# Optimization experiments

Hardware: AMD Instinct MI355X
Metric: run time of the kernel (lower is better)

## Reference

```python
import jax, jax.numpy as jnp
import numpy as np

B, N_HEADS, F_TOK = 8, 12, 768
GRID_H, GRID_W = 32, 32
N_TOK = 1 + GRID_H * GRID_W  # 1025 (readout token + patches)
F_HEAD = F_TOK // N_HEADS    # 64
NUM_DIST = (2 * GRID_H - 1) * (2 * GRID_W - 1) + 3  # 3972


def _build_relpos_index(gh, gw):
    # BEiT-style relative position index with 3 extra slots for the readout token
    coords = np.stack(np.meshgrid(np.arange(gh), np.arange(gw), indexing='ij'))  # (2, gh, gw)
    flat = coords.reshape(2, -1)                                                 # (2, gh*gw)
    rel = flat[:, :, None] - flat[:, None, :]                                    # (2, P, P)
    rel = rel.transpose(1, 2, 0).astype(np.int64)                                # (P, P, 2)
    rel[:, :, 0] += gh - 1
    rel[:, :, 1] += gw - 1
    rel[:, :, 0] *= 2 * gw - 1
    rpi = rel.sum(-1)                                                            # (P, P)
    n = 1 + gh * gw
    nd = (2 * gh - 1) * (2 * gw - 1) + 3
    idx = np.zeros((n, n), dtype=np.int32)
    idx[1:, 1:] = rpi
    idx[0, :] = nd - 3  # readout -> all
    idx[:, 0] = nd - 2  # all -> readout
    idx[0, 0] = nd - 1  # readout -> readout
    return idx


def setup_inputs() -> dict:
    key = jax.random.key(0)
    ks = jax.random.split(key, 7)
    tokens = jax.random.normal(ks[0], (B, N_TOK, F_TOK), dtype=jnp.float32)
    qkv_w = jax.random.normal(ks[1], (3 * F_TOK, F_TOK), dtype=jnp.float32) * 0.02
    q_bias = jax.random.normal(ks[2], (1, N_HEADS, 1, F_HEAD), dtype=jnp.float32) * 0.02
    v_bias = jax.random.normal(ks[3], (1, N_HEADS, 1, F_HEAD), dtype=jnp.float32) * 0.02
    relpos_table = jax.random.normal(ks[4], (NUM_DIST, N_HEADS), dtype=jnp.float32) * 0.02
    proj_w = jax.random.normal(ks[5], (F_TOK, F_TOK), dtype=jnp.float32) * 0.02
    proj_b = jax.random.normal(ks[6], (F_TOK,), dtype=jnp.float32) * 0.02
    relpos_index = jnp.asarray(_build_relpos_index(GRID_H, GRID_W))  # (N, N) int32
    return {
        'tokens': tokens, 'qkv_w': qkv_w, 'q_bias': q_bias, 'v_bias': v_bias,
        'relpos_table': relpos_table, 'proj_w': proj_w, 'proj_b': proj_b,
        'relpos_index': relpos_index, 'patch_h': GRID_H, 'patch_w': GRID_W,
    }


def reference(tokens, qkv_w, q_bias, v_bias, relpos_table, proj_w, proj_b,
              relpos_index, patch_h, patch_w):
    b, n, f_tok = tokens.shape
    # qkv projection (no bias): (B, N, 3F) -> (3, B, H, N, f)
    qkv = tokens @ qkv_w.T
    qkv = qkv.reshape(b, n, 3, N_HEADS, F_HEAD).transpose(2, 0, 3, 1, 4)
    q, k, v = qkv[0], qkv[1], qkv[2]
    q = (q + q_bias) * (F_HEAD ** -0.5)
    v = v + v_bias
    # attention scores: (B, H, N, N)
    attn = jnp.einsum('bhnf,bhmf->bhnm', q, k)
    # relative position bias gather: (N, N, H) -> (H, N, N)
    bias = relpos_table[relpos_index].transpose(2, 0, 1)
    attn = attn + bias[None]
    w = jax.nn.softmax(attn, axis=-1)
    out = jnp.einsum('bhnm,bhmf->bhnf', w, v)
    out = out.transpose(0, 2, 1, 3).reshape(b, n, N_HEADS * F_HEAD)
    return out @ proj_w.T + proj_b
```

## Files before the change

kernel.cpp:

```cpp
#include <hip/hip_runtime.h>

#define B_ 8
#define NH 12
#define NTOK 1025
#define FT 768
#define MROWS (B_*NTOK)
#define NPAD2 1088
#define CH2 34
#define NQT 36
#define NTT 34
#define NRT18 18
#define LOG2E 1.44269504089f

typedef __bf16 bf16x8 __attribute__((ext_vector_type(8)));
typedef __bf16 bf16x2 __attribute__((ext_vector_type(2)));
typedef float floatx4 __attribute__((ext_vector_type(4)));
typedef float floatx16 __attribute__((ext_vector_type(16)));
typedef int intx4 __attribute__((ext_vector_type(4)));

__device__ __forceinline__ void async_ld16(const void* gp, void* lp) {
  __builtin_amdgcn_global_load_lds(
      (const __attribute__((address_space(1))) void*)gp,
      (__attribute__((address_space(3))) void*)lp, 16, 0, 0);
}

__global__ __launch_bounds__(256) void cvt_bf16(const float* __restrict__ src,
                                                __bf16* __restrict__ dst, int n4) {
  int i = blockIdx.x * 256 + threadIdx.x;
  if (i >= n4) return;
  float4 v = ((const float4*)src)[i];
  __bf16 o[4] = {(__bf16)v.x, (__bf16)v.y, (__bf16)v.z, (__bf16)v.w};
  *(uint2*)(dst + 4 * (size_t)i) = *(uint2*)o;
}

__global__ __launch_bounds__(256) void bias_gather_t(
    const int* __restrict__ idx, const float* __restrict__ table,
    __bf16* __restrict__ Bb) {
  const int qt = blockIdx.x, tt = blockIdx.y;
  const int t = threadIdx.x;
  const int lane = t & 63, w = t >> 6;
  const int l31 = lane & 31, hb = lane >> 5;
  int qrow = qt * 32 + l31; if (qrow > NTOK - 1) qrow = NTOK - 1;
  int ids[16]; bool ok[16];
#pragma unroll
  for (int j = 0; j < 16; ++j) {
    const int token = tt * 32 + (j & 3) + 8 * (j >> 2) + 4 * hb;
    ok[j] = token < NTOK;
    ids[j] = ok[j] ? idx[qrow * NTOK + token] : 0;
  }
#pragma unroll
  for (int g = 0; g < 3; ++g) {
    const int h = w + g * 4;
    __bf16 v[16];
#pragma unroll
    for (int j = 0; j < 16; ++j)
      v[j] = ok[j] ? (__bf16)(table[ids[j] * NH + h] * LOG2E) : (__bf16)(-1e30f);
    uint4* dst = (uint4*)(Bb + (((size_t)h * NQT + qt) * NTT + tt) * 1024 + lane * 16);
    dst[0] = ((uint4*)v)[0];
    dst[1] = ((uint4*)v)[1];
  }
}

__device__ __forceinline__ void gemm128_pipe(
    const __bf16* __restrict__ A, const __bf16* __restrict__ W,
    int m0, int n0, int M, __bf16* At, __bf16* Bt, floatx4 acc[4][4]) {
  const int tid = threadIdx.x, wave = tid >> 6, lane = tid & 63;
  const int l = lane & 15, qd = lane >> 4;
  const int wr = wave >> 1, wc = wave & 1;
  const int srow = lane >> 2, sg = lane & 3;
  const int r0 = wave * 32 + srow, r1 = r0 + 16;
  int gm0 = m0 + r0; if (gm0 >= M) gm0 = M - 1;
  int gm1 = m0 + r1; if (gm1 >= M) gm1 = M - 1;
  const int sw0 = (sg ^ (r0 & 3)) * 8;
  const __bf16* gA0 = A + (size_t)gm0 * FT + sw0;
  const __bf16* gA1 = A + (size_t)gm1 * FT + sw0;
  const __bf16* gB0 = W + (size_t)(n0 + r0) * FT + sw0;
  const __bf16* gB1 = W + (size_t)(n0 + r1) * FT + sw0;
  const int woff = wave * 32 * 32;
  const int fsw = (qd ^ (l & 3)) * 8;

  auto issue = [&](int k, int buf) {
    __bf16* a = At + buf * 4096 + woff;
    __bf16* b = Bt + buf * 4096 + woff;
    async_ld16(gA0 + k * 32, a);
    async_ld16(gA1 + k * 32, a + 512);
    async_ld16(gB0 + k * 32, b);
    async_ld16(gB1 + k * 32, b + 512);
  };
  auto step = [&](int buf) {
    __builtin_amdgcn_s_barrier();
    const __bf16* ab = At + buf * 4096;
    const __bf16* bb = Bt + buf * 4096;
    bf16x8 aF[4], bF[4];
#pragma unroll
    for (int t = 0; t < 4; ++t)
      aF[t] = *(const bf16x8*)(ab + (wr * 64 + t * 16 + l) * 32 + fsw);
#pragma unroll
    for (int u = 0; u < 4; ++u)
      bF[u] = *(const bf16x8*)(bb + (wc * 64 + u * 16 + l) * 32 + fsw);
#pragma unroll
    for (int t = 0; t < 4; ++t)
#pragma unroll
      for (int u = 0; u < 4; ++u)
        acc[t][u] = __builtin_amdgcn_mfma_f32_16x16x32_bf16(aF[t], bF[u], acc[t][u], 0, 0, 0);
  };

  issue(0, 0);
  int bk = 0;
  for (int k = 0; k < 23; ++k) {
    int bn = bk + 1; if (bn == 3) bn = 0;
    issue(k + 1, bn);
    __builtin_amdgcn_s_waitcnt(0x0F74);
    step(bk);
    bk = bn;
  }
  __builtin_amdgcn_s_waitcnt(0x0F70);
  step(bk);
}

__global__ __launch_bounds__(256) void qkv_gemm128(
    const __bf16* __restrict__ tokens, const __bf16* __restrict__ qkvw,
    const float* __restrict__ qbias, const float* __restrict__ vbias,
    __bf16* __restrict__ Qb, __bf16* __restrict__ Kc, __bf16* __restrict__ Vc) {
  __shared__ __bf16 At[3 * 4096], Bt[3 * 4096];
  const int u0 = blockIdx.x;
  const int c = u0 & 7, q0 = u0 >> 3;
  const int mi = (q0 / 18) * 8 + c, ni = q0 % 18;
  if (mi >= 65) return;
  const int m0 = mi * 128, n0 = ni * 128;
  const int tid = threadIdx.x, wave = tid >> 6, lane = tid & 63;
  const int l = lane & 15, qd = lane >> 4;
  const int wr = wave >> 1, wc = wave & 1;
  floatx4 acc[4][4];
#pragma unroll
  for (int t = 0; t < 4; ++t)
#pragma unroll
    for (int u = 0; u < 4; ++u) acc[t][u] = (floatx4){0.f, 0.f, 0.f, 0.f};
  gemm128_pipe(tokens, qkvw, m0, n0, MROWS, At, Bt, acc);

  const int which = (n0 / FT);
  const int nrem0 = n0 - which * FT;
#pragma unroll
  for (int u = 0; u < 4; ++u) {
    const int rem = nrem0 + wc * 64 + u * 16 + l;
    const int h = rem >> 6, f = rem & 63;
    const float qb = (which == 0) ? qbias[h * 64 + f] : 0.f;
    const float vb = (which == 2) ? vbias[h * 64 + f] : 0.f;
#pragma unroll
    for (int t = 0; t < 4; ++t) {
#pragma unroll
      for (int r = 0; r < 4; ++r) {
        const int gm = m0 + wr * 64 + t * 16 + qd * 4 + r;
        if (gm >= MROWS) continue;
        const int b = gm / NTOK;
        const int tok = gm - b * NTOK;
        const size_t bh = (size_t)(b * NH + h);
        float v = acc[t][u][r];
        if (which == 0) {
          Qb[(bh * NPAD2 + tok) * 64 + f] = (__bf16)((v + qb) * (0.125f * LOG2E));
        } else if (which == 1) {
          const size_t e = ((size_t)(bh * CH2 + (tok >> 5))) * 2048 +
                           (((f >> 3) * 32 + (tok & 31)) << 3) + (f & 7);
          Kc[e] = (__bf16)v;
        } else {
          const size_t e = ((size_t)(bh * CH2 + (tok >> 5))) * 2048 +
                           (((((tok >> 3) & 3) * 64 + f)) << 3) + (tok & 7);
          Vc[e] = (__bf16)(v + vb);
        }
      }
    }
  }
}

__global__ __launch_bounds__(256) void proj_gemm128(
    const __bf16* __restrict__ Ao, const __bf16* __restrict__ projw,
    const float* __restrict__ projb, float* __restrict__ out) {
  __shared__ __bf16 At[3 * 4096], Bt[3 * 4096];
  const int u0 = blockIdx.x;
  const int c = u0 & 7, q0 = u0 >> 3;
  const int mi = (q0 / 6) * 8 + c, ni = q0 % 6;
  if (mi >= 65) return;
  const int m0 = mi * 128, n0 = ni * 128;
  const int tid = threadIdx.x, wave = tid >> 6, lane = tid & 63;
  const int l = lane & 15, qd = lane >> 4;
  const int wr = wave >> 1, wc = wave & 1;
  floatx4 acc[4][4];
#pragma unroll
  for (int t = 0; t < 4; ++t)
#pragma unroll
    for (int u = 0; u < 4; ++u) acc[t][u] = (floatx4){0.f, 0.f, 0.f, 0.f};
  gemm128_pipe(Ao, projw, m0, n0, MROWS, At, Bt, acc);
#pragma unroll
  for (int u = 0; u < 4; ++u) {
    const int gn = n0 + wc * 64 + u * 16 + l;
    const float pb = projb[gn];
#pragma unroll
    for (int t = 0; t < 4; ++t)
#pragma unroll
      for (int r = 0; r < 4; ++r) {
        const int gm = m0 + wr * 64 + t * 16 + qd * 4 + r;
        if (gm < MROWS) out[(size_t)gm * FT + gn] = acc[t][u][r] + pb;
      }
  }
}

__global__ __launch_bounds__(128) void attn_flash(
    const __bf16* __restrict__ Qb, const __bf16* __restrict__ Kc,
    const __bf16* __restrict__ Vc, const __bf16* __restrict__ Bb,
    __bf16* __restrict__ Ao) {
  __shared__ __bf16 Kl[3][2048], Vl[3][2048];
  const int bh = blockIdx.x;
  const int rt = blockIdx.y;
  const int h = bh % NH, b = bh / NH;
  const int wave = threadIdx.x >> 6, lane = threadIdx.x & 63;
  const int l31 = lane & 31, hb = lane >> 5;
  const int qt = rt * 2 + wave;
  int qrow = qt * 32 + l31; if (qrow > NTOK - 1) qrow = NTOK - 1;

  bf16x8 qf[4];
  {
    const __bf16* Qp = Qb + ((size_t)bh * NPAD2 + qrow) * 64 + hb * 8;
#pragma unroll
    for (int d = 0; d < 4; ++d) qf[d] = *(const bf16x8*)(Qp + d * 16);
  }

  floatx16 o0, o1;
#pragma unroll
  for (int j = 0; j < 16; ++j) { o0[j] = 0.f; o1[j] = 0.f; }
  float lsum = 0.f;

  const __bf16* KVg = (wave ? Vc : Kc) + (size_t)bh * CH2 * 2048;
  const __bf16* Bg = Bb + ((size_t)h * NQT + qt) * NTT * 1024 + lane * 16;

  auto issue = [&](int c, int buf) {
    const __bf16* src = KVg + (size_t)c * 2048 + lane * 8;
    __bf16* dst = wave ? Vl[buf] : Kl[buf];
#pragma unroll
    for (int ii = 0; ii < 4; ++ii) async_ld16(src + ii * 512, dst + ii * 512);
  };

  issue(0, 0);
  bf16x8 bc0 = *(const bf16x8*)(Bg);
  bf16x8 bc1 = *(const bf16x8*)(Bg + 8);
  int buf = 0;
  for (int c = 0; c < CH2; ++c) {
    int nbuf = buf + 1; if (nbuf == 3) nbuf = 0;
    bf16x8 bn0 = bc0, bn1 = bc1;
    if (c + 1 < CH2) {
      issue(c + 1, nbuf);
      bn0 = *(const bf16x8*)(Bg + (size_t)(c + 1) * 1024);
      bn1 = *(const bf16x8*)(Bg + (size_t)(c + 1) * 1024 + 8);
      __builtin_amdgcn_s_waitcnt(0x0F76);
    } else {
      __builtin_amdgcn_s_waitcnt(0x0F70);
    }
    __builtin_amdgcn_s_barrier();

    floatx16 st;
#pragma unroll
    for (int j = 0; j < 16; ++j) st[j] = 0.f;
#pragma unroll
    for (int dk = 0; dk < 4; ++dk) {
      bf16x8 a = *(const bf16x8*)(Kl[buf] + ((dk * 2 + hb) * 32 + l31) * 8);
      st = __builtin_amdgcn_mfma_f32_32x32x16_bf16(a, qf[dk], st, 0, 0, 0);
    }
    float e[16];
#pragma unroll
    for (int j = 0; j < 16; ++j) {
      const float bj = (float)(j < 8 ? bc0[j] : bc1[j - 8]);
      e[j] = __builtin_amdgcn_exp2f(st[j] + bj);
      lsum += e[j];
    }
    int pk[8];
#pragma unroll
    for (int j2 = 0; j2 < 8; ++j2) {
      bf16x2 pr = {(__bf16)e[2 * j2], (__bf16)e[2 * j2 + 1]};
      pk[j2] = __builtin_bit_cast(int, pr);
    }
#pragma unroll
    for (int ks = 0; ks < 2; ++ks) {
      const int r01a = pk[4 * ks + 0], r01b = pk[4 * ks + 1];
      const int r23a = pk[4 * ks + 2], r23b = pk[4 * ks + 3];
      const int t01a = __shfl_xor(r01a, 32), t01b = __shfl_xor(r01b, 32);
      const int t23a = __shfl_xor(r23a, 32), t23b = __shfl_xor(r23b, 32);
      intx4 fi;
      fi[0] = hb ? t23a : r01a;
      fi[1] = hb ? t23b : r01b;
      fi[2] = hb ? r23a : t01a;
      fi[3] = hb ? r23b : t01b;
      bf16x8 pb = __builtin_bit_cast(bf16x8, fi);
      bf16x8 va0 = *(const bf16x8*)(Vl[buf] + ((ks * 2 + hb) * 64 + l31) * 8);
      bf16x8 va1 = *(const bf16x8*)(Vl[buf] + ((ks * 2 + hb) * 64 + 32 + l31) * 8);
      o0 = __builtin_amdgcn_mfma_f32_32x32x16_bf16(va0, pb, o0, 0, 0, 0);
      o1 = __builtin_amdgcn_mfma_f32_32x32x16_bf16(va1, pb, o1, 0, 0, 0);
    }
    bc0 = bn0; bc1 = bn1;
    buf = nbuf;
  }

  const float ltot = lsum + __shfl_xor(lsum, 32);
  const float rinv = 1.0f / ltot;
  const int tok = rt * 64 + wave * 32 + l31;
  if (tok < NTOK) {
    __bf16* op = Ao + ((size_t)b * NTOK + tok) * FT + h * 64;
#pragma unroll
    for (int ft = 0; ft < 2; ++ft) {
#pragma unroll
      for (int jg = 0; jg < 4; ++jg) {
        const int f = ft * 32 + jg * 8 + hb * 4;
        __bf16 v4[4];
#pragma unroll
        for (int q = 0; q < 4; ++q) {
          const float ov = ft ? o1[jg * 4 + q] : o0[jg * 4 + q];
          v4[q] = (__bf16)(ov * rinv);
        }
        *(uint2*)(op + f) = *(uint2*)v4;
      }
    }
  }
}

extern "C" void kernel_launch(void* const* d_in, const int* in_sizes, int n_in,
                              void* d_out, int out_size, void* d_ws, size_t ws_size,
                              hipStream_t stream) {
  (void)in_sizes; (void)n_in; (void)out_size; (void)ws_size;
  const float* tokens = (const float*)d_in[0];
  const float* qkvw   = (const float*)d_in[1];
  const float* qbias  = (const float*)d_in[2];
  const float* vbias  = (const float*)d_in[3];
  const float* table  = (const float*)d_in[4];
  const float* projw  = (const float*)d_in[5];
  const float* projb  = (const float*)d_in[6];
  const int*   rpidx  = (const int*)d_in[7];
  float* out = (float*)d_out;
  char* ws = (char*)d_ws;

  const size_t QB2 = (size_t)B_ * NH * NPAD2 * 64 * 2;
  const size_t BBT = (size_t)NH * NQT * NTT * 1024 * 2;
  const size_t AOB = (size_t)MROWS * FT * 2;
  const size_t WQB = (size_t)3 * FT * FT * 2;
  __bf16* Qb = (__bf16*)(ws);
  __bf16* Kc = (__bf16*)(ws + QB2);
  __bf16* Vc = (__bf16*)(ws + 2 * QB2);
  __bf16* Bb = (__bf16*)(ws + 3 * QB2);
  __bf16* Tb = (__bf16*)(ws + 3 * QB2 + BBT);
  __bf16* Ao = Tb;
  __bf16* Wq = (__bf16*)(ws + 3 * QB2 + BBT + AOB);
  __bf16* Wp = (__bf16*)(ws + 3 * QB2 + BBT + AOB + WQB);

  cvt_bf16<<<(MROWS * FT / 4 + 255) / 256, 256, 0, stream>>>(tokens, Tb, MROWS * FT / 4);
  cvt_bf16<<<(3 * FT * FT / 4 + 255) / 256, 256, 0, stream>>>(qkvw, Wq, 3 * FT * FT / 4);
  cvt_bf16<<<(FT * FT / 4 + 255) / 256, 256, 0, stream>>>(projw, Wp, FT * FT / 4);
  bias_gather_t<<<dim3(NQT, NTT), 256, 0, stream>>>(rpidx, table, Bb);
  qkv_gemm128<<<8 * 9 * 18, 256, 0, stream>>>(Tb, Wq, qbias, vbias, Qb, Kc, Vc);
  attn_flash<<<dim3(B_ * NH, NRT18), 128, 0, stream>>>(Qb, Kc, Vc, Bb, Ao);
  proj_gemm128<<<8 * 9 * 6, 256, 0, stream>>>(Ao, Wp, projb, out);
}
```

Measured before the change: 273.1 us.

## Load GEMM A-operand directly to registers and merge the three conversion kernels

The GEMM helper now reads the A operand (activations) straight from global memory into MFMA fragment registers, double-buffered in registers, and stages only the weight tile through LDS. This halves shared memory per block and removes the LDS round trip for A, which could raise occupancy. The cost is uncoalesced, redundant global loads of A across waves in the same row. Separately, the three fp32-to-bf16 conversion launches are merged into one kernel to cut launch overhead.

```diff
diff --git a/kernel.cpp b/kernel.cpp
--- a/kernel.cpp
+++ b/kernel.cpp
@@ -24,13 +24,18 @@
       (__attribute__((address_space(3))) void*)lp, 16, 0, 0);
 }
 
-__global__ __launch_bounds__(256) void cvt_bf16(const float* __restrict__ src,
-                                                __bf16* __restrict__ dst, int n4) {
+__global__ __launch_bounds__(256) void cvt3_bf16(
+    const float* __restrict__ s0, __bf16* __restrict__ d0, int n0,
+    const float* __restrict__ s1, __bf16* __restrict__ d1, int n1,
+    const float* __restrict__ s2, __bf16* __restrict__ d2, int n2) {
   int i = blockIdx.x * 256 + threadIdx.x;
-  if (i >= n4) return;
-  float4 v = ((const float4*)src)[i];
+  const float* s; __bf16* d;
+  if (i < n0) { s = s0; d = d0; }
+  else if (i < n0 + n1) { i -= n0; s = s1; d = d1; }
+  else { i -= n0 + n1; if (i >= n2) return; s = s2; d = d2; }
+  float4 v = ((const float4*)s)[i];
   __bf16 o[4] = {(__bf16)v.x, (__bf16)v.y, (__bf16)v.z, (__bf16)v.w};
-  *(uint2*)(dst + 4 * (size_t)i) = *(uint2*)o;
+  *(uint2*)(d + 4 * (size_t)i) = *(uint2*)o;
 }
 
 __global__ __launch_bounds__(256) void bias_gather_t(
@@ -61,68 +66,85 @@
   }
 }
 
-__device__ __forceinline__ void gemm128_pipe(
+__device__ __forceinline__ void gemm128_ad(
     const __bf16* __restrict__ A, const __bf16* __restrict__ W,
-    int m0, int n0, int M, __bf16* At, __bf16* Bt, floatx4 acc[4][4]) {
+    int m0, int n0, int M, __bf16* Bt, floatx4 acc[4][4]) {
   const int tid = threadIdx.x, wave = tid >> 6, lane = tid & 63;
   const int l = lane & 15, qd = lane >> 4;
   const int wr = wave >> 1, wc = wave & 1;
   const int srow = lane >> 2, sg = lane & 3;
   const int r0 = wave * 32 + srow, r1 = r0 + 16;
-  int gm0 = m0 + r0; if (gm0 >= M) gm0 = M - 1;
-  int gm1 = m0 + r1; if (gm1 >= M) gm1 = M - 1;
   const int sw0 = (sg ^ (r0 & 3)) * 8;
-  const __bf16* gA0 = A + (size_t)gm0 * FT + sw0;
-  const __bf16* gA1 = A + (size_t)gm1 * FT + sw0;
   const __bf16* gB0 = W + (size_t)(n0 + r0) * FT + sw0;
   const __bf16* gB1 = W + (size_t)(n0 + r1) * FT + sw0;
-  const int woff = wave * 32 * 32;
+  const int woff = wave * 1024;
   const int fsw = (qd ^ (l & 3)) * 8;
-
-  auto issue = [&](int k, int buf) {
-    __bf16* a = At + buf * 4096 + woff;
-    __bf16* b = Bt + buf * 4096 + woff;
-    async_ld16(gA0 + k * 32, a);
-    async_ld16(gA1 + k * 32, a + 512);
-    async_ld16(gB0 + k * 32, b);
-    async_ld16(gB1 + k * 32, b + 512);
-  };
-  auto step = [&](int buf) {
-    __builtin_amdgcn_s_barrier();
-    const __bf16* ab = At + buf * 4096;
-    const __bf16* bb = Bt + buf * 4096;
-    bf16x8 aF[4], bF[4];
-#pragma unroll
-    for (int t = 0; t < 4; ++t)
-      aF[t] = *(const bf16x8*)(ab + (wr * 64 + t * 16 + l) * 32 + fsw);
-#pragma unroll
-    for (int u = 0; u < 4; ++u)
-      bF[u] = *(const bf16x8*)(bb + (wc * 64 + u * 16 + l) * 32 + fsw);
-#pragma unroll
-    for (int t = 0; t < 4; ++t)
-#pragma unroll
-      for (int u = 0; u < 4; ++u)
-        acc[t][u] = __builtin_amdgcn_mfma_f32_16x16x32_bf16(aF[t], bF[u], acc[t][u], 0, 0, 0);
-  };
-
-  issue(0, 0);
+  const __bf16* gA[4];
+#pragma unroll
+  for (int t = 0; t < 4; ++t) {
+    int gm = m0 + wr * 64 + t * 16 + l;
+    if (gm >= M) gm = M - 1;
+    gA[t] = A + (size_t)gm * FT + qd * 8;
+  }
+
+  bf16x8 aF[4], aN[4];
+#pragma unroll
+  for (int t = 0; t < 4; ++t) aF[t] = *(const bf16x8*)(gA[t]);
+  {
+    __bf16* b = Bt + woff;
+    async_ld16(gB0, b);
+    async_ld16(gB1, b + 512);
+  }
+
   int bk = 0;
   for (int k = 0; k < 23; ++k) {
     int bn = bk + 1; if (bn == 3) bn = 0;
-    issue(k + 1, bn);
-    __builtin_amdgcn_s_waitcnt(0x0F74);
-    step(bk);
+    {
+      __bf16* b = Bt + bn * 4096 + woff;
+      async_ld16(gB0 + (k + 1) * 32, b);
+      async_ld16(gB1 + (k + 1) * 32, b + 512);
+    }
+#pragma unroll
+    for (int t = 0; t < 4; ++t) aN[t] = *(const bf16x8*)(gA[t] + (k + 1) * 32);
+    __builtin_amdgcn_s_waitcnt(0x0F76);
+    __builtin_amdgcn_s_barrier();
+    {
+      const __bf16* bb = Bt + bk * 4096;
+      bf16x8 bF[4];
+#pragma unroll
+      for (int u = 0; u < 4; ++u)
+        bF[u] = *(const bf16x8*)(bb + (wc * 64 + u * 16 + l) * 32 + fsw);
+#pragma unroll
+      for (int t = 0; t < 4; ++t)
+#pragma unroll
+        for (int u = 0; u < 4; ++u)
+          acc[t][u] = __builtin_amdgcn_mfma_f32_16x16x32_bf16(aF[t], bF[u], acc[t][u], 0, 0, 0);
+    }
+#pragma unroll
+    for (int t = 0; t < 4; ++t) aF[t] = aN[t];
     bk = bn;
   }
   __builtin_amdgcn_s_waitcnt(0x0F70);
-  step(bk);
+  __builtin_amdgcn_s_barrier();
+  {
+    const __bf16* bb = Bt + bk * 4096;
+    bf16x8 bF[4];
+#pragma unroll
+    for (int u = 0; u < 4; ++u)
+      bF[u] = *(const bf16x8*)(bb + (wc * 64 + u * 16 + l) * 32 + fsw);
+#pragma unroll
+    for (int t = 0; t < 4; ++t)
+#pragma unroll
+      for (int u = 0; u < 4; ++u)
+        acc[t][u] = __builtin_amdgcn_mfma_f32_16x16x32_bf16(aF[t], bF[u], acc[t][u], 0, 0, 0);
+  }
 }
 
 __global__ __launch_bounds__(256) void qkv_gemm128(
     const __bf16* __restrict__ tokens, const __bf16* __restrict__ qkvw,
     const float* __restrict__ qbias, const float* __restrict__ vbias,
     __bf16* __restrict__ Qb, __bf16* __restrict__ Kc, __bf16* __restrict__ Vc) {
-  __shared__ __bf16 At[3 * 4096], Bt[3 * 4096];
+  __shared__ __bf16 Bt[3 * 4096];
   const int u0 = blockIdx.x;
   const int c = u0 & 7, q0 = u0 >> 3;
   const int mi = (q0 / 18) * 8 + c, ni = q0 % 18;
@@ -136,7 +158,7 @@
   for (int t = 0; t < 4; ++t)
 #pragma unroll
     for (int u = 0; u < 4; ++u) acc[t][u] = (floatx4){0.f, 0.f, 0.f, 0.f};
-  gemm128_pipe(tokens, qkvw, m0, n0, MROWS, At, Bt, acc);
+  gemm128_ad(tokens, qkvw, m0, n0, MROWS, Bt, acc);
 
   const int which = (n0 / FT);
   const int nrem0 = n0 - which * FT;
@@ -175,7 +197,7 @@
 __global__ __launch_bounds__(256) void proj_gemm128(
     const __bf16* __restrict__ Ao, const __bf16* __restrict__ projw,
     const float* __restrict__ projb, float* __restrict__ out) {
-  __shared__ __bf16 At[3 * 4096], Bt[3 * 4096];
+  __shared__ __bf16 Bt[3 * 4096];
   const int u0 = blockIdx.x;
   const int c = u0 & 7, q0 = u0 >> 3;
   const int mi = (q0 / 6) * 8 + c, ni = q0 % 6;
@@ -189,7 +211,7 @@
   for (int t = 0; t < 4; ++t)
 #pragma unroll
     for (int u = 0; u < 4; ++u) acc[t][u] = (floatx4){0.f, 0.f, 0.f, 0.f};
-  gemm128_pipe(Ao, projw, m0, n0, MROWS, At, Bt, acc);
+  gemm128_ad(Ao, projw, m0, n0, MROWS, Bt, acc);
 #pragma unroll
   for (int u = 0; u < 4; ++u) {
     const int gn = n0 + wc * 64 + u * 16 + l;
@@ -348,9 +370,9 @@
   __bf16* Wq = (__bf16*)(ws + 3 * QB2 + BBT + AOB);
   __bf16* Wp = (__bf16*)(ws + 3 * QB2 + BBT + AOB + WQB);
 
-  cvt_bf16<<<(MROWS * FT / 4 + 255) / 256, 256, 0, stream>>>(tokens, Tb, MROWS * FT / 4);
-  cvt_bf16<<<(3 * FT * FT / 4 + 255) / 256, 256, 0, stream>>>(qkvw, Wq, 3 * FT * FT / 4);
-  cvt_bf16<<<(FT * FT / 4 + 255) / 256, 256, 0, stream>>>(projw, Wp, FT * FT / 4);
+  const int n0 = MROWS * FT / 4, n1 = 3 * FT * FT / 4, n2 = FT * FT / 4;
+  cvt3_bf16<<<(n0 + n1 + n2 + 255) / 256, 256, 0, stream>>>(
+      tokens, Tb, n0, qkvw, Wq, n1, projw, Wp, n2);
   bias_gather_t<<<dim3(NQT, NTT), 256, 0, stream>>>(rpidx, table, Bb);
   qkv_gemm128<<<8 * 9 * 18, 256, 0, stream>>>(Tb, Wq, qbias, vbias, Qb, Kc, Vc);
   attn_flash<<<dim3(B_ * NH, NRT18), 128, 0, stream>>>(Qb, Kc, Vc, Bb, Ao);
```

Result: slower. 306.2 us (+12.1%).

## Deepen async prefetch to two stages ahead and merge fp32-to-bf16 conversion launches

Applied to the files above, without the earlier changes.

The GEMM and attention loops now issue global-to-LDS loads two iterations ahead over four LDS buffers instead of one ahead over three, with matching waitcnt values, so more memory latency can be hidden behind MFMA work. The three conversion kernels are merged into a single launch that picks its source by index range, removing two launch overheads. The cost is larger LDS use per block, which may lower occupancy, plus more register pressure in attention from holding extra bias registers.

```diff
diff --git a/kernel.cpp b/kernel.cpp
--- a/kernel.cpp
+++ b/kernel.cpp
@@ -24,13 +24,18 @@
       (__attribute__((address_space(3))) void*)lp, 16, 0, 0);
 }
 
-__global__ __launch_bounds__(256) void cvt_bf16(const float* __restrict__ src,
-                                                __bf16* __restrict__ dst, int n4) {
+__global__ __launch_bounds__(256) void cvt3_bf16(
+    const float* __restrict__ s0, __bf16* __restrict__ d0, int n0,
+    const float* __restrict__ s1, __bf16* __restrict__ d1, int n1,
+    const float* __restrict__ s2, __bf16* __restrict__ d2, int n2) {
   int i = blockIdx.x * 256 + threadIdx.x;
-  if (i >= n4) return;
-  float4 v = ((const float4*)src)[i];
+  const float* s; __bf16* d;
+  if (i < n0) { s = s0; d = d0; }
+  else if (i < n0 + n1) { i -= n0; s = s1; d = d1; }
+  else { i -= n0 + n1; if (i >= n2) return; s = s2; d = d2; }
+  float4 v = ((const float4*)s)[i];
   __bf16 o[4] = {(__bf16)v.x, (__bf16)v.y, (__bf16)v.z, (__bf16)v.w};
-  *(uint2*)(dst + 4 * (size_t)i) = *(uint2*)o;
+  *(uint2*)(d + 4 * (size_t)i) = *(uint2*)o;
 }
 
 __global__ __launch_bounds__(256) void bias_gather_t(
@@ -76,7 +81,7 @@
   const __bf16* gA1 = A + (size_t)gm1 * FT + sw0;
   const __bf16* gB0 = W + (size_t)(n0 + r0) * FT + sw0;
   const __bf16* gB1 = W + (size_t)(n0 + r1) * FT + sw0;
-  const int woff = wave * 32 * 32;
+  const int woff = wave * 1024;
   const int fsw = (qd ^ (l & 3)) * 8;
 
   auto issue = [&](int k, int buf) {
@@ -106,23 +111,28 @@
   };
 
   issue(0, 0);
+  issue(1, 1);
   int bk = 0;
-  for (int k = 0; k < 23; ++k) {
-    int bn = bk + 1; if (bn == 3) bn = 0;
-    issue(k + 1, bn);
-    __builtin_amdgcn_s_waitcnt(0x0F74);
+  for (int k = 0; k < 24; ++k) {
+    if (k + 2 < 24) {
+      int bi = bk + 2; if (bi >= 4) bi -= 4;
+      issue(k + 2, bi);
+      __builtin_amdgcn_s_waitcnt(0x0F78);
+    } else if (k == 22) {
+      __builtin_amdgcn_s_waitcnt(0x0F74);
+    } else {
+      __builtin_amdgcn_s_waitcnt(0x0F70);
+    }
     step(bk);
-    bk = bn;
-  }
-  __builtin_amdgcn_s_waitcnt(0x0F70);
-  step(bk);
+    bk = (bk + 1) & 3;
+  }
 }
 
 __global__ __launch_bounds__(256) void qkv_gemm128(
     const __bf16* __restrict__ tokens, const __bf16* __restrict__ qkvw,
     const float* __restrict__ qbias, const float* __restrict__ vbias,
     __bf16* __restrict__ Qb, __bf16* __restrict__ Kc, __bf16* __restrict__ Vc) {
-  __shared__ __bf16 At[3 * 4096], Bt[3 * 4096];
+  __shared__ __bf16 At[4 * 4096], Bt[4 * 4096];
   const int u0 = blockIdx.x;
   const int c = u0 & 7, q0 = u0 >> 3;
   const int mi = (q0 / 18) * 8 + c, ni = q0 % 18;
@@ -175,7 +185,7 @@
 __global__ __launch_bounds__(256) void proj_gemm128(
     const __bf16* __restrict__ Ao, const __bf16* __restrict__ projw,
     const float* __restrict__ projb, float* __restrict__ out) {
-  __shared__ __bf16 At[3 * 4096], Bt[3 * 4096];
+  __shared__ __bf16 At[4 * 4096], Bt[4 * 4096];
   const int u0 = blockIdx.x;
   const int c = u0 & 7, q0 = u0 >> 3;
   const int mi = (q0 / 6) * 8 + c, ni = q0 % 6;
@@ -208,7 +218,7 @@
     const __bf16* __restrict__ Qb, const __bf16* __restrict__ Kc,
     const __bf16* __restrict__ Vc, const __bf16* __restrict__ Bb,
     __bf16* __restrict__ Ao) {
-  __shared__ __bf16 Kl[3][2048], Vl[3][2048];
+  __shared__ __bf16 Kl[4][2048], Vl[4][2048];
   const int bh = blockIdx.x;
   const int rt = blockIdx.y;
   const int h = bh % NH, b = bh / NH;
@@ -239,20 +249,21 @@
     for (int ii = 0; ii < 4; ++ii) async_ld16(src + ii * 512, dst + ii * 512);
   };
 
+  bf16x8 ba[3], bz[3];
   issue(0, 0);
-  bf16x8 bc0 = *(const bf16x8*)(Bg);
-  bf16x8 bc1 = *(const bf16x8*)(Bg + 8);
+  ba[0] = *(const bf16x8*)(Bg);
+  bz[0] = *(const bf16x8*)(Bg + 8);
+  issue(1, 1);
+  ba[1] = *(const bf16x8*)(Bg + 1024);
+  bz[1] = *(const bf16x8*)(Bg + 1024 + 8);
   int buf = 0;
   for (int c = 0; c < CH2; ++c) {
-    int nbuf = buf + 1; if (nbuf == 3) nbuf = 0;
-    bf16x8 bn0 = bc0, bn1 = bc1;
-    if (c + 1 < CH2) {
-      issue(c + 1, nbuf);
-      bn0 = *(const bf16x8*)(Bg + (size_t)(c + 1) * 1024);
-      bn1 = *(const bf16x8*)(Bg + (size_t)(c + 1) * 1024 + 8);
-      __builtin_amdgcn_s_waitcnt(0x0F76);
-    } else {
-      __builtin_amdgcn_s_waitcnt(0x0F70);
+    {
+      int cc = c + 2; if (cc > CH2 - 1) cc = CH2 - 1;
+      issue(cc, (buf + 2) & 3);
+      ba[2] = *(const bf16x8*)(Bg + (size_t)cc * 1024);
+      bz[2] = *(const bf16x8*)(Bg + (size_t)cc * 1024 + 8);
+      __builtin_amdgcn_s_waitcnt(0x0F7C);
     }
     __builtin_amdgcn_s_barrier();
 
@@ -267,7 +278,7 @@
     float e[16];
 #pragma unroll
     for (int j = 0; j < 16; ++j) {
-      const float bj = (float)(j < 8 ? bc0[j] : bc1[j - 8]);
+      const float bj = (float)(j < 8 ? ba[0][j] : bz[0][j - 8]);
       e[j] = __builtin_amdgcn_exp2f(st[j] + bj);
       lsum += e[j];
     }
@@ -294,9 +305,11 @@
       o0 = __builtin_amdgcn_mfma_f32_32x32x16_bf16(va0, pb, o0, 0, 0, 0);
       o1 = __builtin_amdgcn_mfma_f32_32x32x16_bf16(va1, pb, o1, 0, 0, 0);
     }
-    bc0 = bn0; bc1 = bn1;
-    buf = nbuf;
-  }
+    ba[0] = ba[1]; ba[1] = ba[2];
+    bz[0] = bz[1]; bz[1] = bz[2];
+    buf = (buf + 1) & 3;
+  }
+  __builtin_amdgcn_s_waitcnt(0x0F70);
 
   const float ltot = lsum + __shfl_xor(lsum, 32);
   const float rinv = 1.0f / ltot;
@@ -348,9 +361,9 @@
   __bf16* Wq = (__bf16*)(ws + 3 * QB2 + BBT + AOB);
   __bf16* Wp = (__bf16*)(ws + 3 * QB2 + BBT + AOB + WQB);
 
-  cvt_bf16<<<(MROWS * FT / 4 + 255) / 256, 256, 0, stream>>>(tokens, Tb, MROWS * FT / 4);
-  cvt_bf16<<<(3 * FT * FT / 4 + 255) / 256, 256, 0, stream>>>(qkvw, Wq, 3 * FT * FT / 4);
-  cvt_bf16<<<(FT * FT / 4 + 255) / 256, 256, 0, stream>>>(projw, Wp, FT * FT / 4);
+  const int n0 = MROWS * FT / 4, n1 = 3 * FT * FT / 4, n2 = FT * FT / 4;
+  cvt3_bf16<<<(n0 + n1 + n2 + 255) / 256, 256, 0, stream>>>(
+      tokens, Tb, n0, qkvw, Wq, n1, projw, Wp, n2);
   bias_gather_t<<<dim3(NQT, NTT), 256, 0, stream>>>(rpidx, table, Bb);
   qkv_gemm128<<<8 * 9 * 18, 256, 0, stream>>>(Tb, Wq, qbias, vbias, Qb, Kc, Vc);
   attn_flash<<<dim3(B_ * NH, NRT18), 128, 0, stream>>>(Qb, Kc, Vc, Bb, Ao);
```

Result: slower. 289.4 us (+6.0%).
